# Performance work log

Hardware: AMD Instinct MI355X
Metric: run time of the kernel (lower is better)

The kernel has to match this reference:

```python
import jax, jax.numpy as jnp
import numpy as np

SIZE_SUBMAP = 1024          # points per submap (module global in repo)
RATIO = 0.5                 # CONFIG['Detector']['ratio']
K_POS = int(SIZE_SUBMAP * RATIO)  # 512
K = 32                      # self.k, fps ratio = K / K_POS
B = 2048                    # number of submaps in batch


def fps_single(pts, k):
    """Deterministic farthest point sampling (start at index 0). pts: [n,3] -> [k] int indices."""
    min_d = jnp.sum((pts - pts[0]) ** 2, axis=-1)  # [n]

    def step(min_d, _):
        idx = jnp.argmax(min_d)
        d2 = jnp.sum((pts - pts[idx]) ** 2, axis=-1)
        return jnp.minimum(min_d, d2), idx

    _, idxs = jax.lax.scan(step, min_d, None, length=k - 1)
    return jnp.concatenate([jnp.zeros((1,), dtype=idxs.dtype), idxs])


def setup_inputs() -> dict:
    key = jax.random.key(0)
    ks = jax.random.split(key, 8)
    n = B * SIZE_SUBMAP
    x = jax.random.normal(ks[0], (n, 32), jnp.float32)
    pos = jax.random.normal(ks[1], (n, 3), jnp.float32) * 10.0
    batch = jnp.repeat(jnp.arange(B, dtype=jnp.int32), SIZE_SUBMAP)
    # MLP([32,16,8]) -> Linear(8,1) -> Softplus
    W1 = jax.random.normal(ks[2], (32, 16), jnp.float32) / np.sqrt(32.0)
    b1 = jnp.zeros((16,), jnp.float32)
    W2 = jax.random.normal(ks[3], (16, 8), jnp.float32) / np.sqrt(16.0)
    b2 = jnp.zeros((8,), jnp.float32)
    W3 = jax.random.normal(ks[4], (8, 1), jnp.float32) / np.sqrt(8.0)
    b3 = jnp.zeros((1,), jnp.float32)
    return {"x": x, "pos": pos, "batch": batch,
            "W1": W1, "b1": b1, "W2": W2, "b2": b2, "W3": W3, "b3": b3}


def reference(x, pos, batch, W1, b1, W2, b2, W3, b3):
    bsz = batch.shape[0] // SIZE_SUBMAP  # static batch_size (= batch.max()+1)
    # small per-point MLP + Softplus score
    h = jax.nn.relu(x @ W1 + b1)
    h = jax.nn.relu(h @ W2 + b2)
    s = jax.nn.softplus(h @ W3 + b3)          # [B*N, 1]
    x_batch = s.reshape(bsz, -1)               # [B, N]
    pos_b = pos.reshape(bsz, -1, 3)            # [B, N, 3]
    # distance of xy-coords to submap center
    dist = jnp.linalg.norm(pos_b[..., :2], axis=-1)     # [B, N]
    # k_pos closest points (topk of -dist)
    _, idx1 = jax.lax.top_k(-dist, K_POS)               # [B, K_POS]
    pos_sel = jnp.take_along_axis(pos_b, idx1[..., None], axis=1)  # [B, K_POS, 3]
    # batched farthest point sampling, K points per submap (within-batch indices)
    key_idx = jax.vmap(lambda p: fps_single(p, K))(pos_sel)        # [B, K]
    original_indices = jnp.take_along_axis(idx1, key_idx, axis=1)  # [B, K]
    weights = jnp.take_along_axis(x_batch, original_indices, axis=1)  # [B, K]
    return weights, original_indices
```

## Files before the change

kernel.cpp:

```cpp
#include <hip/hip_runtime.h>
#include <math.h>
#include <stdint.h>

#define N_PTS 1024
#define K_FPS 32

typedef unsigned long long u64;
typedef unsigned int u32;

__device__ __forceinline__ u64 shfl_xor_u64(u64 v, int mask) {
    return __shfl_xor(v, mask, 64);
}

__device__ __forceinline__ int imax2(int a, int b) { return a > b ? a : b; }

template<int CTRL, int RM>
__device__ __forceinline__ int dpp_upd(int v) {
    return __builtin_amdgcn_update_dpp(0, v, CTRL, RM, 0xf, true);
}

template<int M>
__device__ __forceinline__ u64 xshfl(u64 v) {
    if constexpr (M == 32) {
        return shfl_xor_u64(v, 32);
    } else {
        u32 lo = (u32)v, hi = (u32)(v >> 32);
        if constexpr (M == 1) {
            lo = (u32)dpp_upd<0xB1, 0xf>((int)lo);
            hi = (u32)dpp_upd<0xB1, 0xf>((int)hi);
        } else if constexpr (M == 2) {
            lo = (u32)dpp_upd<0x4E, 0xf>((int)lo);
            hi = (u32)dpp_upd<0x4E, 0xf>((int)hi);
        } else {
            constexpr int imm = (M << 10) | 0x1F;
            lo = (u32)__builtin_amdgcn_ds_swizzle((int)lo, imm);
            hi = (u32)__builtin_amdgcn_ds_swizzle((int)hi, imm);
        }
        return ((u64)hi << 32) | lo;
    }
}

template<int J>
__device__ __forceinline__ void intra8(u64 key[8], int L, int k) {
    #pragma unroll
    for (int r = 0; r < 8; ++r) {
        if ((r & J) == 0) {
            const int r2 = r | J;
            int p = (L << 3) | r;
            bool up = ((p & k) == 0);
            u64 a = key[r], c = key[r2];
            bool sw = a < c;
            u64 lo2 = sw ? a : c;
            u64 hi2 = sw ? c : a;
            key[r]  = up ? lo2 : hi2;
            key[r2] = up ? hi2 : lo2;
        }
    }
}

template<int M>
__device__ __forceinline__ void cross8(u64 key[8], int L, int k) {
    bool low = ((L & M) == 0);
    bool up  = ((L & (k >> 3)) == 0);
    bool sel = (low == up);
    #pragma unroll
    for (int r = 0; r < 8; ++r) {
        u64 o = xshfl<M>(key[r]);
        key[r] = ((key[r] < o) == sel) ? key[r] : o;
    }
}

__device__ float mlp_point(const float* __restrict__ xr,
                           const float* __restrict__ W1, const float* __restrict__ b1,
                           const float* __restrict__ W2, const float* __restrict__ b2,
                           const float* __restrict__ W3, const float* __restrict__ b3)
{
#pragma clang fp contract(fast)
    float h1[16];
    #pragma unroll
    for (int j = 0; j < 16; ++j) h1[j] = b1[j];
    #pragma unroll
    for (int i = 0; i < 32; i += 4) {
        float4 v = *(const float4*)(xr + i);
        float xv[4] = {v.x, v.y, v.z, v.w};
        #pragma unroll
        for (int q = 0; q < 4; ++q) {
            #pragma unroll
            for (int j = 0; j < 16; ++j)
                h1[j] += xv[q] * W1[(i + q) * 16 + j];
        }
    }
    #pragma unroll
    for (int j = 0; j < 16; ++j) h1[j] = fmaxf(h1[j], 0.0f);

    float h2[8];
    #pragma unroll
    for (int j = 0; j < 8; ++j) {
        float a = b2[j];
        #pragma unroll
        for (int i = 0; i < 16; ++i) a += h1[i] * W2[i * 8 + j];
        h2[j] = fmaxf(a, 0.0f);
    }
    float v = b3[0];
    #pragma unroll
    for (int i = 0; i < 8; ++i) v += h2[i] * W3[i];

    return fmaxf(v, 0.0f) + log1pf(expf(-fabsf(v)));
}

__global__ __launch_bounds__(128) void sortfps_kernel(
    const float* __restrict__ pos,
    const float* __restrict__ x,
    const float* __restrict__ W1, const float* __restrict__ b1,
    const float* __restrict__ W2, const float* __restrict__ b2,
    const float* __restrict__ W3, const float* __restrict__ b3,
    float* __restrict__ out_w,
    float* __restrict__ out_idx,
    int B)
{
#pragma clang fp contract(off)
    const int t    = threadIdx.x;
    const int lane = t & 63;
    const int wv   = t >> 6;
    const int b    = blockIdx.x;

    __shared__ __attribute__((aligned(16))) float spts[N_PTS * 3];
    __shared__ u64 xch[512];

    if (b >= B) return;

    const float* pb = pos + (size_t)b * N_PTS * 3;

    float4 f4[6];
    {
        const float4* pb4 = (const float4*)pb + (size_t)t * 6;
        #pragma unroll
        for (int i = 0; i < 6; ++i) f4[i] = pb4[i];
        float4* sp4 = (float4*)spts + t * 6;
        #pragma unroll
        for (int i = 0; i < 6; ++i) sp4[i] = f4[i];
    }
    const float* f = (const float*)&f4[0];

    u64 key[8];
    #pragma unroll
    for (int r = 0; r < 8; ++r) {
        int p = (t << 3) | r;
        float xc = f[r * 3 + 0];
        float yc = f[r * 3 + 1];
        float xx = xc * xc, yy = yc * yc;
        float d = sqrtf(xx + yy);
        key[r] = ((u64)__float_as_uint(d) << 32) | (u32)p;
    }

    intra8<1>(key, t, 2);
    intra8<2>(key, t, 4);  intra8<1>(key, t, 4);
    intra8<4>(key, t, 8);  intra8<2>(key, t, 8);  intra8<1>(key, t, 8);

    cross8<1>(key, t, 16);
    intra8<4>(key, t, 16); intra8<2>(key, t, 16); intra8<1>(key, t, 16);

    cross8<2>(key, t, 32); cross8<1>(key, t, 32);
    intra8<4>(key, t, 32); intra8<2>(key, t, 32); intra8<1>(key, t, 32);

    cross8<4>(key, t, 64); cross8<2>(key, t, 64); cross8<1>(key, t, 64);
    intra8<4>(key, t, 64); intra8<2>(key, t, 64); intra8<1>(key, t, 64);

    cross8<8>(key, t, 128); cross8<4>(key, t, 128); cross8<2>(key, t, 128);
    cross8<1>(key, t, 128);
    intra8<4>(key, t, 128); intra8<2>(key, t, 128); intra8<1>(key, t, 128);

    cross8<16>(key, t, 256); cross8<8>(key, t, 256); cross8<4>(key, t, 256);
    cross8<2>(key, t, 256);  cross8<1>(key, t, 256);
    intra8<4>(key, t, 256); intra8<2>(key, t, 256); intra8<1>(key, t, 256);

    cross8<32>(key, t, 512); cross8<16>(key, t, 512); cross8<8>(key, t, 512);
    cross8<4>(key, t, 512);  cross8<2>(key, t, 512);  cross8<1>(key, t, 512);
    intra8<4>(key, t, 512); intra8<2>(key, t, 512); intra8<1>(key, t, 512);

    if (wv == 1) {
        #pragma unroll
        for (int r = 0; r < 8; ++r) xch[r * 64 + lane] = key[r];
    }
    __syncthreads();
    if (wv == 1) return;

    #pragma unroll
    for (int r = 0; r < 8; ++r) {
        u64 o = xch[r * 64 + lane];
        key[r] = key[r] < o ? key[r] : o;
    }
    cross8<32>(key, t, 1024); cross8<16>(key, t, 1024); cross8<8>(key, t, 1024);
    cross8<4>(key, t, 1024);  cross8<2>(key, t, 1024);  cross8<1>(key, t, 1024);
    intra8<4>(key, t, 1024); intra8<2>(key, t, 1024); intra8<1>(key, t, 1024);


    float px[8], py[8], pz[8], pidx[8], mind[8];
    #pragma unroll
    for (int r = 0; r < 8; ++r) {
        int o = (int)(u32)key[r];
        const float* sp = &spts[o * 3];
        px[r] = sp[0]; py[r] = sp[1]; pz[r] = sp[2];
        pidx[r] = (float)o;
    }

    float* ob = out_idx + (size_t)b * K_FPS;
    int o0 = __builtin_amdgcn_readfirstlane((int)(u32)key[0]);
    float wx = spts[o0 * 3], wy = spts[o0 * 3 + 1], wz = spts[o0 * 3 + 2];
    float acc = (float)o0;

    #pragma unroll
    for (int r = 0; r < 8; ++r) {
        float dx = px[r] - wx, dy = py[r] - wy, dz = pz[r] - wz;
        float u0 = dx * dx, u1 = dy * dy, u2 = dz * dz;
        mind[r] = (u0 + u1) + u2;
    }

    for (int it = 1; it < K_FPS; ++it) {
        float v4[4], i4[4], x4[4], y4[4], z4[4];
        #pragma unroll
        for (int q = 0; q < 4; ++q) {
            bool g = mind[2 * q + 1] > mind[2 * q];
            v4[q] = g ? mind[2 * q + 1] : mind[2 * q];
            i4[q] = g ? pidx[2 * q + 1] : pidx[2 * q];
            x4[q] = g ? px[2 * q + 1] : px[2 * q];
            y4[q] = g ? py[2 * q + 1] : py[2 * q];
            z4[q] = g ? pz[2 * q + 1] : pz[2 * q];
        }
        bool s01 = v4[1] > v4[0];
        float va = s01 ? v4[1] : v4[0], ia = s01 ? i4[1] : i4[0];
        float xa = s01 ? x4[1] : x4[0], ya = s01 ? y4[1] : y4[0];
        float za = s01 ? z4[1] : z4[0];
        bool s23 = v4[3] > v4[2];
        float vb = s23 ? v4[3] : v4[2], ib = s23 ? i4[3] : i4[2];
        float xb = s23 ? x4[3] : x4[2], yb = s23 ? y4[3] : y4[2];
        float zb = s23 ? z4[3] : z4[2];
        bool sab = vb > va;
        float bv = sab ? vb : va, bi = sab ? ib : ia;
        float bx = sab ? xb : xa, by = sab ? yb : ya, bz = sab ? zb : za;

        int bvi = __float_as_int(bv);
        int g = bvi;
        g = imax2(g, dpp_upd<0x111, 0xf>(g));
        g = imax2(g, dpp_upd<0x112, 0xf>(g));
        g = imax2(g, dpp_upd<0x114, 0xf>(g));
        g = imax2(g, dpp_upd<0x118, 0xf>(g));
        g = imax2(g, dpp_upd<0x142, 0xa>(g));
        g = imax2(g, dpp_upd<0x143, 0xc>(g));
        int gmax = __builtin_amdgcn_readlane(g, 63);

        u64 mask = __ballot(bvi == gmax);
        int W = __ffsll((unsigned long long)mask) - 1;
        wx = __uint_as_float(__builtin_amdgcn_readlane(__float_as_uint(bx), W));
        wy = __uint_as_float(__builtin_amdgcn_readlane(__float_as_uint(by), W));
        wz = __uint_as_float(__builtin_amdgcn_readlane(__float_as_uint(bz), W));
        float wi = __uint_as_float(__builtin_amdgcn_readlane(__float_as_uint(bi), W));
        if (lane == it) acc = wi;

        #pragma unroll
        for (int r = 0; r < 8; ++r) {
            float dx = px[r] - wx, dy = py[r] - wy, dz = pz[r] - wz;
            float u0 = dx * dx, u1 = dy * dy, u2 = dz * dz;
            float d2 = (u0 + u1) + u2;
            mind[r] = fminf(mind[r], d2);
        }
    }

    if (lane < K_FPS) {
        ob[lane] = acc;
        int orig = (int)acc;
        const float* xr = x + ((size_t)b * N_PTS + (size_t)orig) * 32;
        float w = mlp_point(xr, W1, b1, W2, b2, W3, b3);
        out_w[(size_t)b * K_FPS + lane] = w;
    }
}

extern "C" void kernel_launch(void* const* d_in, const int* in_sizes, int n_in,
                              void* d_out, int out_size, void* d_ws, size_t ws_size,
                              hipStream_t stream) {
    const float* x   = (const float*)d_in[0];
    const float* pos = (const float*)d_in[1];
    const float* W1 = (const float*)d_in[3];
    const float* b1 = (const float*)d_in[4];
    const float* W2 = (const float*)d_in[5];
    const float* b2 = (const float*)d_in[6];
    const float* W3 = (const float*)d_in[7];
    const float* b3 = (const float*)d_in[8];

    const int B = in_sizes[2] / N_PTS;
    float* out_w = (float*)d_out;
    float* out_i = (float*)d_out + (size_t)B * K_FPS;

    sortfps_kernel<<<B, 128, 0, stream>>>(
        pos, x, W1, b1, W2, b2, W3, b3, out_w, out_i, B);
}
```

Measured before the change: 368.0 us.

## Use DPP/permlane cross-lane ops in sort and LDS lookup for FPS winner

```diff
diff --git a/kernel.cpp b/kernel.cpp
--- a/kernel.cpp
+++ b/kernel.cpp
@@ -7,10 +7,7 @@
 
 typedef unsigned long long u64;
 typedef unsigned int u32;
-
-__device__ __forceinline__ u64 shfl_xor_u64(u64 v, int mask) {
-    return __shfl_xor(v, mask, 64);
-}
+typedef unsigned int uint2v __attribute__((ext_vector_type(2)));
 
 __device__ __forceinline__ int imax2(int a, int b) { return a > b ? a : b; }
 
@@ -20,24 +17,41 @@
 }
 
 template<int M>
-__device__ __forceinline__ u64 xshfl(u64 v) {
-    if constexpr (M == 32) {
-        return shfl_xor_u64(v, 32);
+__device__ __forceinline__ u32 xlane(u32 x, int lane) {
+    if constexpr (M == 1) {
+        return (u32)dpp_upd<0xB1, 0xf>((int)x);
+    } else if constexpr (M == 2) {
+        return (u32)dpp_upd<0x4E, 0xf>((int)x);
+    } else if constexpr (M == 4) {
+        u32 a = (u32)dpp_upd<0x104, 0xf>((int)x);
+        u32 b = (u32)dpp_upd<0x114, 0xf>((int)x);
+        return (lane & 4) ? b : a;
+    } else if constexpr (M == 8) {
+        u32 a = (u32)dpp_upd<0x108, 0xf>((int)x);
+        u32 b = (u32)dpp_upd<0x118, 0xf>((int)x);
+        return (lane & 8) ? b : a;
+    } else if constexpr (M == 16) {
+#if __has_builtin(__builtin_amdgcn_permlane16_swap)
+        uint2v r = __builtin_amdgcn_permlane16_swap(x, x, false, false);
+        return (lane & 16) ? r.x : r.y;
+#else
+        return (u32)__builtin_amdgcn_ds_swizzle((int)x, (16 << 10) | 0x1F);
+#endif
     } else {
-        u32 lo = (u32)v, hi = (u32)(v >> 32);
-        if constexpr (M == 1) {
-            lo = (u32)dpp_upd<0xB1, 0xf>((int)lo);
-            hi = (u32)dpp_upd<0xB1, 0xf>((int)hi);
-        } else if constexpr (M == 2) {
-            lo = (u32)dpp_upd<0x4E, 0xf>((int)lo);
-            hi = (u32)dpp_upd<0x4E, 0xf>((int)hi);
-        } else {
-            constexpr int imm = (M << 10) | 0x1F;
-            lo = (u32)__builtin_amdgcn_ds_swizzle((int)lo, imm);
-            hi = (u32)__builtin_amdgcn_ds_swizzle((int)hi, imm);
-        }
-        return ((u64)hi << 32) | lo;
-    }
+#if __has_builtin(__builtin_amdgcn_permlane32_swap)
+        uint2v r = __builtin_amdgcn_permlane32_swap(x, x, false, false);
+        return (lane & 32) ? r.x : r.y;
+#else
+        return (u32)__shfl_xor((int)x, 32, 64);
+#endif
+    }
+}
+
+template<int M>
+__device__ __forceinline__ u64 xshfl(u64 v, int lane) {
+    u32 lo = xlane<M>((u32)v, lane);
+    u32 hi = xlane<M>((u32)(v >> 32), lane);
+    return ((u64)hi << 32) | lo;
 }
 
 template<int J>
@@ -60,12 +74,13 @@
 
 template<int M>
 __device__ __forceinline__ void cross8(u64 key[8], int L, int k) {
+    const int lane = L & 63;
     bool low = ((L & M) == 0);
     bool up  = ((L & (k >> 3)) == 0);
     bool sel = (low == up);
     #pragma unroll
     for (int r = 0; r < 8; ++r) {
-        u64 o = xshfl<M>(key[r]);
+        u64 o = xshfl<M>(key[r], lane);
         key[r] = ((key[r] < o) == sel) ? key[r] : o;
     }
 }
@@ -108,7 +123,7 @@
     return fmaxf(v, 0.0f) + log1pf(expf(-fabsf(v)));
 }
 
-__global__ __launch_bounds__(128) void sortfps_kernel(
+__global__ __launch_bounds__(128, 4) void sortfps_kernel(
     const float* __restrict__ pos,
     const float* __restrict__ x,
     const float* __restrict__ W1, const float* __restrict__ b1,
@@ -204,7 +219,6 @@
         pidx[r] = (float)o;
     }
 
-    float* ob = out_idx + (size_t)b * K_FPS;
     int o0 = __builtin_amdgcn_readfirstlane((int)(u32)key[0]);
     float wx = spts[o0 * 3], wy = spts[o0 * 3 + 1], wz = spts[o0 * 3 + 2];
     float acc = (float)o0;
@@ -217,27 +231,19 @@
     }
 
     for (int it = 1; it < K_FPS; ++it) {
-        float v4[4], i4[4], x4[4], y4[4], z4[4];
+        float v4[4], i4[4];
         #pragma unroll
         for (int q = 0; q < 4; ++q) {
             bool g = mind[2 * q + 1] > mind[2 * q];
             v4[q] = g ? mind[2 * q + 1] : mind[2 * q];
             i4[q] = g ? pidx[2 * q + 1] : pidx[2 * q];
-            x4[q] = g ? px[2 * q + 1] : px[2 * q];
-            y4[q] = g ? py[2 * q + 1] : py[2 * q];
-            z4[q] = g ? pz[2 * q + 1] : pz[2 * q];
         }
         bool s01 = v4[1] > v4[0];
         float va = s01 ? v4[1] : v4[0], ia = s01 ? i4[1] : i4[0];
-        float xa = s01 ? x4[1] : x4[0], ya = s01 ? y4[1] : y4[0];
-        float za = s01 ? z4[1] : z4[0];
         bool s23 = v4[3] > v4[2];
         float vb = s23 ? v4[3] : v4[2], ib = s23 ? i4[3] : i4[2];
-        float xb = s23 ? x4[3] : x4[2], yb = s23 ? y4[3] : y4[2];
-        float zb = s23 ? z4[3] : z4[2];
         bool sab = vb > va;
         float bv = sab ? vb : va, bi = sab ? ib : ia;
-        float bx = sab ? xb : xa, by = sab ? yb : ya, bz = sab ? zb : za;
 
         int bvi = __float_as_int(bv);
         int g = bvi;
@@ -251,10 +257,9 @@
 
         u64 mask = __ballot(bvi == gmax);
         int W = __ffsll((unsigned long long)mask) - 1;
-        wx = __uint_as_float(__builtin_amdgcn_readlane(__float_as_uint(bx), W));
-        wy = __uint_as_float(__builtin_amdgcn_readlane(__float_as_uint(by), W));
-        wz = __uint_as_float(__builtin_amdgcn_readlane(__float_as_uint(bz), W));
         float wi = __uint_as_float(__builtin_amdgcn_readlane(__float_as_uint(bi), W));
+        int wo = (int)wi;
+        wx = spts[wo * 3]; wy = spts[wo * 3 + 1]; wz = spts[wo * 3 + 2];
         if (lane == it) acc = wi;
 
         #pragma unroll
@@ -267,7 +272,7 @@
     }
 
     if (lane < K_FPS) {
-        ob[lane] = acc;
+        out_idx[(size_t)b * K_FPS + lane] = acc;
         int orig = (int)acc;
         const float* xr = x + ((size_t)b * N_PTS + (size_t)orig) * 32;
         float w = mlp_point(xr, W1, b1, W2, b2, W3, b3);
```

Measured after the change: 355.1 us. 1.04x faster.
